# Kernel optimization log

Hardware: AMD Instinct MI355X
Metric: run time of the kernel (lower is better)

## Reference

```python
import jax, jax.numpy as jnp
import numpy as np

N_NODES = 40962
N_EDGES = 245760
K = 10  # gaussian kernels
D = 2   # pseudo-coordinate dim
EPS = 1e-15


def gmm_conv(x, edge_index, pseudo, g, mu, sigma, root, bias):
    """PyG GMMConv with aggr='mean', root_weight=True.
    x: [N, Cin], edge_index: [2, E] (row 0 = source j, row 1 = target i),
    pseudo: [E, D], g: [Cin, K*Cout], mu/sigma: [K, D], root: [Cin, Cout], bias: [Cout].
    """
    src, dst = edge_index[0], edge_index[1]
    E = pseudo.shape[0]
    # Gaussian mixture edge weights: [E, K]
    diff = pseudo[:, None, :] - mu[None, :, :]                     # [E, K, D]
    w = jnp.exp(jnp.sum(-0.5 * diff * diff / (EPS + sigma[None] ** 2), axis=-1))
    xj = x[src]                                                    # [E, Cin] gather
    y = (xj @ g).reshape(E, K, -1)                                 # [E, K, Cout]
    msg = jnp.sum(y * w[:, :, None], axis=1)                       # [E, Cout]
    agg = jax.ops.segment_sum(msg, dst, num_segments=N_NODES)      # scatter-add
    deg = jax.ops.segment_sum(jnp.ones((E,), x.dtype), dst, num_segments=N_NODES)
    agg = agg / jnp.maximum(deg, 1.0)[:, None]                     # mean aggregation
    return agg + x @ root + bias


def setup_inputs() -> dict:
    key = jax.random.key(0)
    ks = jax.random.split(key, 20)
    Cin, Ch, Cout = 64, 64, 128
    sc = lambda fan: 1.0 / np.sqrt(fan)
    inp = {
        "x": jax.random.normal(ks[0], (N_NODES, Cin), jnp.float32),
        "edge_index": jax.random.randint(ks[1], (2, N_EDGES), 0, N_NODES, jnp.int32),
        "pseudo": jax.random.uniform(ks[2], (N_EDGES, D), jnp.float32),
        # conv1: Cin -> Ch
        "g1": jax.random.normal(ks[3], (Cin, K * Ch), jnp.float32) * sc(Cin),
        "mu1": jax.random.uniform(ks[4], (K, D), jnp.float32),
        "sigma1": jax.random.uniform(ks[5], (K, D), jnp.float32) + 0.5,
        "root1": jax.random.normal(ks[6], (Cin, Ch), jnp.float32) * sc(Cin),
        "b1": jnp.zeros((Ch,), jnp.float32),
        # conv2: Ch -> Cout
        "g2": jax.random.normal(ks[7], (Ch, K * Cout), jnp.float32) * sc(Ch),
        "mu2": jax.random.uniform(ks[8], (K, D), jnp.float32),
        "sigma2": jax.random.uniform(ks[9], (K, D), jnp.float32) + 0.5,
        "root2": jax.random.normal(ks[10], (Ch, Cout), jnp.float32) * sc(Ch),
        "b2": jnp.zeros((Cout,), jnp.float32),
        # shortcut: Cin -> Cout (size_in != size_out)
        "gs": jax.random.normal(ks[11], (Cin, K * Cout), jnp.float32) * sc(Cin),
        "mus": jax.random.uniform(ks[12], (K, D), jnp.float32),
        "sigmas": jax.random.uniform(ks[13], (K, D), jnp.float32) + 0.5,
        "roots": jax.random.normal(ks[14], (Cin, Cout), jnp.float32) * sc(Cin),
        "bs": jnp.zeros((Cout,), jnp.float32),
    }
    return inp


def reference(x, edge_index, pseudo, g1, mu1, sigma1, root1, b1,
              g2, mu2, sigma2, root2, b2, gs, mus, sigmas, roots, bs):
    h = gmm_conv(x, edge_index, pseudo, g1, mu1, sigma1, root1, b1)
    h = jax.nn.relu(h)
    y = gmm_conv(h, edge_index, pseudo, g2, mu2, sigma2, root2, b2)
    x_s = gmm_conv(x, edge_index, pseudo, gs, mus, sigmas, roots, bs)
    return jax.nn.relu(y + x_s)
```

## Files before the change

### kernel.cpp

```cpp
#include <hip/hip_runtime.h>
#include <hip/hip_bf16.h>

using bf16 = __hip_bfloat16;
typedef __attribute__((ext_vector_type(8))) short short8;
typedef __attribute__((ext_vector_type(4))) float float4v;

#define N_NODES 40962
#define N_EDGES 245760
#define NP      41024
#define KG      10
#define SCAN_B  256
#define NBLK    ((NP + SCAN_B - 1) / SCAN_B)
#define GRID1   (NP / 64)

#define CVT_V   (N_NODES * 64 / 8)
#define CVT_BLK ((CVT_V + 255) / 256)
#define W3_BLK  (N_EDGES / 256)
#define PACK_N  (64 * 704 + 2 * 128 * 704)
#define PACK_BLK (PACK_N / 256)


__device__ __forceinline__ float ldf(const void* p, size_t i, int isf32) {
    return isf32 ? ((const float*)p)[i] : __bfloat162float(((const bf16*)p)[i]);
}
__device__ __forceinline__ float blo(unsigned u) { return __uint_as_float(u << 16); }
__device__ __forceinline__ float bhi(unsigned u) { return __uint_as_float(u & 0xffff0000u); }
__device__ __forceinline__ unsigned pk2(float a, float b) {
    union { bf16 h[2]; unsigned u; } t;
    t.h[0] = __float2bfloat16(a);
    t.h[1] = __float2bfloat16(b);
    return t.u;
}
__device__ __forceinline__ int rfl(int v) { return __builtin_amdgcn_readfirstlane(v); }

__global__ void k_detect_count(const void* x, const int* __restrict__ ei,
                               int* __restrict__ flag, int* __restrict__ deg) {
    if (blockIdx.x == 0) {
        __shared__ int huge_c, zero_even;
        if (threadIdx.x == 0) { huge_c = 0; zero_even = 0; }
        __syncthreads();
        const bf16* xb = (const bf16*)x;
        int lh = 0, lz = 0;
        for (int i = threadIdx.x; i < 8192; i += 256) {
            float v = __bfloat162float(xb[i]);
            if (!(fabsf(v) <= 1e4f)) lh++;
            if ((i & 1) == 0 && v == 0.0f) lz++;
        }
        atomicAdd(&huge_c, lh);
        atomicAdd(&zero_even, lz);
        __syncthreads();
        if (threadIdx.x == 0) flag[0] = (huge_c > 0 || zero_even > 3000) ? 1 : 0;
    } else {
        int e = (blockIdx.x - 1) * 256 + threadIdx.x;
        if (e < N_EDGES) atomicAdd(&deg[ei[N_EDGES + e]], 1);
    }
}

__global__ void k_scan1(const int* __restrict__ deg, int* __restrict__ offs,
                        int* __restrict__ bsum) {
    __shared__ int buf[SCAN_B];
    int t = threadIdx.x, b = blockIdx.x;
    int i = b * SCAN_B + t;
    int v = (i < NP) ? deg[i] : 0;
    buf[t] = v;
    __syncthreads();
    for (int off = 1; off < SCAN_B; off <<= 1) {
        int a = (t >= off) ? buf[t - off] : 0;
        __syncthreads();
        buf[t] += a;
        __syncthreads();
    }
    if (i < NP) offs[i] = buf[t] - v;
    if (t == SCAN_B - 1) bsum[b] = buf[t];
}

__global__ void k_scan3m(int* __restrict__ offs, const int* __restrict__ bsum,
                         const int* __restrict__ deg, int* __restrict__ cur,
                         float* __restrict__ invdeg) {
    __shared__ int buf[256];
    int t = threadIdx.x, b = blockIdx.x;
    int v = (t < NBLK) ? bsum[t] : 0;
    buf[t] = v;
    __syncthreads();
    for (int off = 1; off < 256; off <<= 1) {
        int a = (t >= off) ? buf[t - off] : 0;
        __syncthreads();
        buf[t] += a;
        __syncthreads();
    }
    int bofs = (b > 0) ? buf[b - 1] : 0;
    int total = buf[NBLK - 1];
    int i = b * 256 + t;
    if (i < NP) {
        int o = offs[i] + bofs;
        offs[i] = o;
        cur[i] = o;
        int d = deg[i];
        invdeg[i] = 1.0f / (float)(d > 1 ? d : 1);
    }
    if (i == 0) offs[NP] = total;
}

__global__ void k_fill(const int* __restrict__ ei, int* __restrict__ cur,
                       int* __restrict__ csr) {
    int e = blockIdx.x * 256 + threadIdx.x;
    if (e < N_EDGES) {
        int pos = atomicAdd(&cur[ei[N_EDGES + e]], 1);
        csr[pos] = e;
    }
}

__device__ __forceinline__ void gw_one(float p0, float p1, const void* mu,
                                       const void* sg, int f, float* out) {
#pragma unroll
    for (int k = 0; k < KG; k++) {
        float m0 = ldf(mu, 2 * k + 0, f), m1 = ldf(mu, 2 * k + 1, f);
        float s0 = ldf(sg, 2 * k + 0, f), s1 = ldf(sg, 2 * k + 1, f);
        float d0 = p0 - m0, d1 = p1 - m1;
        float t = -0.5f * (d0 * d0 / (1e-15f + s0 * s0) + d1 * d1 / (1e-15f + s1 * s1));
        out[k] = __expf(t);
    }
}

__device__ __forceinline__ void pack_frag(const void* g, const void* root, int f,
                                          int idx, int Cout, bf16* Bp) {
    int j = idx & 7;
    int lane = (idx >> 3) & 63;
    int rem = idx >> 9;
    int kc = rem % 22;
    int n = rem / 22;
    int col = n * 16 + (lane & 15);
    int k = kc * 32 + (lane >> 4) * 8 + j;
    float v;
    if (k < 512) {
        int cin = k >> 3, kg = k & 7;
        v = ldf(g, (size_t)cin * (KG * Cout) + (size_t)kg * Cout + col, f);
    } else if (k < 640) {
        int jj = k - 512;
        int cin = jj >> 1, kg = 8 + (jj & 1);
        v = ldf(g, (size_t)cin * (KG * Cout) + (size_t)kg * Cout + col, f);
    } else {
        v = ldf(root, (size_t)(k - 640) * Cout + col, f);
    }
    Bp[idx] = __float2bfloat16(v);
}

__global__ void k_prep_all(const void* __restrict__ x, const void* __restrict__ pseudo,
                           const void* mu1, const void* sg1, const void* mu2,
                           const void* sg2, const void* mus, const void* sgs,
                           const void* g1, const void* root1, const void* g2,
                           const void* root2, const void* gs, const void* roots,
                           const int* __restrict__ flag, bf16* __restrict__ Xf,
                           bf16* __restrict__ wab, bf16* __restrict__ w2b,
                           bf16* wt1p, bf16* wt2p, bf16* wtsp) {
    int b = blockIdx.x;
    int tid = threadIdx.x;
    int f = flag[0];
    if (b < CVT_BLK) {
        int i = b * 256 + tid;
        if (i < CVT_V) {
            int node = i >> 3, j = i & 7;
            uint4 u;
            if (f) {
                const float4* xf = (const float4*)x;
                float4 a = xf[2 * i], c = xf[2 * i + 1];
                union { bf16 t[8]; uint4 u; } tt;
                tt.t[0] = __float2bfloat16(a.x); tt.t[1] = __float2bfloat16(a.y);
                tt.t[2] = __float2bfloat16(a.z); tt.t[3] = __float2bfloat16(a.w);
                tt.t[4] = __float2bfloat16(c.x); tt.t[5] = __float2bfloat16(c.y);
                tt.t[6] = __float2bfloat16(c.z); tt.t[7] = __float2bfloat16(c.w);
                u = tt.u;
            } else {
                u = ((const uint4*)x)[i];
            }
            *(uint4*)(Xf + ((size_t)(j >> 2) * NP + node) * 32 + (j & 3) * 8) = u;
        }
    } else if (b < CVT_BLK + W3_BLK) {
        int e = (b - CVT_BLK) * 256 + tid;
        float p0 = ldf(pseudo, (size_t)e * 2 + 0, f);
        float p1 = ldf(pseudo, (size_t)e * 2 + 1, f);
        float o1[KG], o2[KG], os[KG];
        gw_one(p0, p1, mu1, sg1, f, o1);
        gw_one(p0, p1, mu2, sg2, f, o2);
        gw_one(p0, p1, mus, sgs, f, os);
        unsigned* d = (unsigned*)(wab + (size_t)e * 20);
        d[0] = pk2(o1[0], o1[1]); d[1] = pk2(o1[2], o1[3]);
        d[2] = pk2(o1[4], o1[5]); d[3] = pk2(o1[6], o1[7]);
        d[4] = pk2(o1[8], o1[9]);
        d[5] = pk2(os[0], os[1]); d[6] = pk2(os[2], os[3]);
        d[7] = pk2(os[4], os[5]); d[8] = pk2(os[6], os[7]);
        d[9] = pk2(os[8], os[9]);
        unsigned* d2 = (unsigned*)(w2b + (size_t)e * 10);
        d2[0] = pk2(o2[0], o2[1]); d2[1] = pk2(o2[2], o2[3]);
        d2[2] = pk2(o2[4], o2[5]); d2[3] = pk2(o2[6], o2[7]);
        d2[4] = pk2(o2[8], o2[9]);
    } else {
        int idx = (b - CVT_BLK - W3_BLK) * 256 + tid;
        if (idx < 64 * 704) {
            pack_frag(g1, root1, f, idx, 64, wt1p);
        } else if (idx < 64 * 704 + 128 * 704) {
            pack_frag(g2, root2, f, idx - 64 * 704, 128, wt2p);
        } else {
            pack_frag(gs, roots, f, idx - 64 * 704 - 128 * 704, 128, wtsp);
        }
    }
}

__device__ __forceinline__ void store_zf(bf16* Zf, int wid, int lane, const float* a,
                                         float inv) {
    union { bf16 h[8]; uint4 u; } p;
#pragma unroll
    for (int k = 0; k < 8; k++) p.h[k] = __float2bfloat16(a[k] * inv);
    *(uint4*)(Zf + ((size_t)(lane >> 2) * NP + wid) * 32 + (lane & 3) * 8) = p.u;
    *(unsigned*)(Zf + ((size_t)(16 + (lane >> 4)) * NP + wid) * 32 + (lane & 15) * 2) =
        pk2(a[8] * inv, a[9] * inv);
}

__device__ __forceinline__ float ldx_frag(const bf16* X, int src, int lane) {
    return __bfloat162float(X[((size_t)(lane >> 5) * NP + src) * 32 + (lane & 31)]);
}

__device__ __forceinline__ int csr_at(const int* csr, int idx) {
    if (idx > N_EDGES - 1) idx = N_EDGES - 1;
    return rfl(csr[idx]);
}

__global__ void k_gather2(const int* __restrict__ ei, const int* __restrict__ offs,
                          const int* __restrict__ csr, const bf16* __restrict__ wab,
                          const float* __restrict__ invdeg, const bf16* __restrict__ X,
                          bf16* __restrict__ Za, bf16* __restrict__ Zb) {
    int wid = (blockIdx.x * 256 + threadIdx.x) >> 6;
    int lane = threadIdx.x & 63;
    if (wid >= NP) return;
    float aa[KG], ab[KG];
#pragma unroll
    for (int k = 0; k < KG; k++) { aa[k] = 0.0f; ab[k] = 0.0f; }
    int beg = rfl(offs[wid]);
    int end = rfl(offs[wid + 1]);
    int cnt = end - beg;

    int e0 = csr_at(csr, beg + 0);
    int e1 = csr_at(csr, beg + 1);
    int e2 = csr_at(csr, beg + 2);
    int s1 = rfl(ei[e1]);
    const unsigned* wp0 = (const unsigned*)(wab + (size_t)e0 * 20);
    unsigned c0 = wp0[0], c1 = wp0[1], c2 = wp0[2], c3 = wp0[3], c4 = wp0[4];
    unsigned c5 = wp0[5], c6 = wp0[6], c7 = wp0[7], c8 = wp0[8], c9 = wp0[9];
    const unsigned* wp1 = (const unsigned*)(wab + (size_t)e1 * 20);
    unsigned n0 = wp1[0], n1 = wp1[1], n2 = wp1[2], n3 = wp1[3], n4 = wp1[4];
    unsigned n5 = wp1[5], n6 = wp1[6], n7 = wp1[7], n8 = wp1[8], n9 = wp1[9];
    int s0 = rfl(ei[e0]);
    float xv = ldx_frag(X, s0, lane);

    for (int t = 0; t < cnt; ++t) {
        int e3 = csr_at(csr, beg + t + 3);
        int s2 = rfl(ei[e2]);
        const unsigned* wp2 = (const unsigned*)(wab + (size_t)e2 * 20);
        unsigned m0 = wp2[0], m1 = wp2[1], m2 = wp2[2], m3 = wp2[3], m4 = wp2[4];
        unsigned m5 = wp2[5], m6 = wp2[6], m7 = wp2[7], m8 = wp2[8], m9 = wp2[9];
        float xv1 = ldx_frag(X, s1, lane);
        aa[0] += blo(c0) * xv; aa[1] += bhi(c0) * xv;
        aa[2] += blo(c1) * xv; aa[3] += bhi(c1) * xv;
        aa[4] += blo(c2) * xv; aa[5] += bhi(c2) * xv;
        aa[6] += blo(c3) * xv; aa[7] += bhi(c3) * xv;
        aa[8] += blo(c4) * xv; aa[9] += bhi(c4) * xv;
        ab[0] += blo(c5) * xv; ab[1] += bhi(c5) * xv;
        ab[2] += blo(c6) * xv; ab[3] += bhi(c6) * xv;
        ab[4] += blo(c7) * xv; ab[5] += bhi(c7) * xv;
        ab[6] += blo(c8) * xv; ab[7] += bhi(c8) * xv;
        ab[8] += blo(c9) * xv; ab[9] += bhi(c9) * xv;
        e2 = e3; s1 = s2; xv = xv1;
        c0 = n0; c1 = n1; c2 = n2; c3 = n3; c4 = n4;
        c5 = n5; c6 = n6; c7 = n7; c8 = n8; c9 = n9;
        n0 = m0; n1 = m1; n2 = m2; n3 = m3; n4 = m4;
        n5 = m5; n6 = m6; n7 = m7; n8 = m8; n9 = m9;
    }
    float inv = invdeg[wid];
    store_zf(Za, wid, lane, aa, inv);
    store_zf(Zb, wid, lane, ab, inv);
}

__global__ void k_gather(const int* __restrict__ ei, const int* __restrict__ offs,
                         const int* __restrict__ csr, const bf16* __restrict__ w,
                         int wstride, const float* __restrict__ invdeg,
                         const bf16* __restrict__ X, bf16* __restrict__ Z) {
    int wid = (blockIdx.x * 256 + threadIdx.x) >> 6;
    int lane = threadIdx.x & 63;
    if (wid >= NP) return;
    float acc[KG];
#pragma unroll
    for (int k = 0; k < KG; k++) acc[k] = 0.0f;
    int beg = rfl(offs[wid]);
    int end = rfl(offs[wid + 1]);
    int cnt = end - beg;

    int e0 = csr_at(csr, beg + 0);
    int e1 = csr_at(csr, beg + 1);
    int e2 = csr_at(csr, beg + 2);
    int s1 = rfl(ei[e1]);
    const unsigned* wp0 = (const unsigned*)(w + (size_t)e0 * wstride);
    unsigned c0 = wp0[0], c1 = wp0[1], c2 = wp0[2], c3 = wp0[3], c4 = wp0[4];
    const unsigned* wp1 = (const unsigned*)(w + (size_t)e1 * wstride);
    unsigned n0 = wp1[0], n1 = wp1[1], n2 = wp1[2], n3 = wp1[3], n4 = wp1[4];
    int s0 = rfl(ei[e0]);
    float xv = ldx_frag(X, s0, lane);

    for (int t = 0; t < cnt; ++t) {
        int e3 = csr_at(csr, beg + t + 3);
        int s2 = rfl(ei[e2]);
        const unsigned* wp2 = (const unsigned*)(w + (size_t)e2 * wstride);
        unsigned m0 = wp2[0], m1 = wp2[1], m2 = wp2[2], m3 = wp2[3], m4 = wp2[4];
        float xv1 = ldx_frag(X, s1, lane);
        acc[0] += blo(c0) * xv; acc[1] += bhi(c0) * xv;
        acc[2] += blo(c1) * xv; acc[3] += bhi(c1) * xv;
        acc[4] += blo(c2) * xv; acc[5] += bhi(c2) * xv;
        acc[6] += blo(c3) * xv; acc[7] += bhi(c3) * xv;
        acc[8] += blo(c4) * xv; acc[9] += bhi(c4) * xv;
        e2 = e3; s1 = s2; xv = xv1;
        c0 = n0; c1 = n1; c2 = n2; c3 = n3; c4 = n4;
        n0 = m0; n1 = m1; n2 = m2; n3 = m3; n4 = m4;
    }
    store_zf(Z, wid, lane, acc, invdeg[wid]);
}

template <int NT, int MODE>
__device__ __forceinline__ void gemm_body(
    int bid, const bf16* __restrict__ Zf, const bf16* __restrict__ Xf,
    const bf16* __restrict__ Bp, const void* __restrict__ bias, int f,
    const bf16* __restrict__ addsrc, bf16* __restrict__ outb,
    void* __restrict__ outp) {
    constexpr int Cout = NT * 16;
    constexpr int AD = (NT == 8) ? 2 : 4;
    int lane = threadIdx.x & 63;
    int wave = threadIdx.x >> 6;
    int m = lane & 15, quad = lane >> 4;
    int row0 = bid * 64 + wave * 16;

    const bf16* bbase = Bp + (size_t)lane * 8;
    const bf16* arow = Zf + ((size_t)(row0 + m)) * 32 + quad * 8;
    const bf16* xrow = Xf + ((size_t)(row0 + m)) * 32 + quad * 8;

    float4v acc[NT];
#pragma unroll
    for (int n = 0; n < NT; n++) acc[n] = (float4v){0.f, 0.f, 0.f, 0.f};

    short8 apre[AD];
#pragma unroll
    for (int i = 0; i < AD; i++)
        apre[i] = *(const short8*)(arow + (size_t)i * NP * 32);
    short8 bpre[2][NT];
#pragma unroll
    for (int n = 0; n < NT; n++) {
        bpre[0][n] = *(const short8*)(bbase + (size_t)(n * 22 + 0) * 512);
        bpre[1][n] = *(const short8*)(bbase + (size_t)(n * 22 + 1) * 512);
    }

#pragma unroll
    for (int kc = 0; kc < 22; kc++) {
        short8 a = apre[kc % AD];
        int kn = kc + AD;
        if (kn < 22) {
            apre[kc % AD] = (kn < 20)
                ? *(const short8*)(arow + (size_t)kn * NP * 32)
                : *(const short8*)(xrow + (size_t)(kn - 20) * NP * 32);
        }
        short8 bcur[NT];
#pragma unroll
        for (int n = 0; n < NT; n++) bcur[n] = bpre[kc & 1][n];
        if (kc + 2 < 22) {
#pragma unroll
            for (int n = 0; n < NT; n++)
                bpre[kc & 1][n] =
                    *(const short8*)(bbase + (size_t)(n * 22 + kc + 2) * 512);
        }
#pragma unroll
        for (int n = 0; n < NT; n++)
            acc[n] = __builtin_amdgcn_mfma_f32_16x16x32_bf16(a, bcur[n], acc[n], 0, 0, 0);
    }

#pragma unroll
    for (int n = 0; n < NT; n++) {
        int gcol = n * 16 + m;
        float bv = ldf(bias, gcol, f);
#pragma unroll
        for (int r = 0; r < 4; r++) {
            int grow = row0 + quad * 4 + r;
            if (grow >= N_NODES) continue;
            float v = acc[n][r] + bv;
            if (MODE == 0) {
                outb[((size_t)(gcol >> 5) * NP + grow) * 32 + (gcol & 31)] =
                    __float2bfloat16(fmaxf(v, 0.f));
            } else if (MODE == 1) {
                outb[(size_t)grow * Cout + gcol] = __float2bfloat16(v);
            } else {
                size_t oidx = (size_t)grow * Cout + gcol;
                v = fmaxf(v + __bfloat162float(addsrc[oidx]), 0.f);
                if (f) ((float*)outp)[oidx] = v;
                else   ((bf16*)outp)[oidx] = __float2bfloat16(v);
            }
        }
    }
}

__global__ __launch_bounds__(256) void k_gemm_pair(
    const bf16* __restrict__ za, const bf16* __restrict__ zb,
    const bf16* __restrict__ Xf, const bf16* __restrict__ wt1p,
    const bf16* __restrict__ wtsp, const void* __restrict__ b1,
    const void* __restrict__ bs, const int* __restrict__ flag,
    bf16* __restrict__ hf, bf16* __restrict__ ys) {
    int f = flag[0];
    if (blockIdx.x < GRID1)
        gemm_body<4, 0>(blockIdx.x, za, Xf, wt1p, b1, f, nullptr, hf, nullptr);
    else
        gemm_body<8, 1>(blockIdx.x - GRID1, zb, Xf, wtsp, bs, f, nullptr, ys, nullptr);
}

template <int NT, int MODE>
__global__ __launch_bounds__(256) void k_gemm_one(
    const bf16* __restrict__ Zf, const bf16* __restrict__ Xf,
    const bf16* __restrict__ Bp, const void* __restrict__ bias,
    const int* __restrict__ flag, const bf16* __restrict__ addsrc,
    bf16* __restrict__ outb, void* __restrict__ outp) {
    gemm_body<NT, MODE>(blockIdx.x, Zf, Xf, Bp, bias, flag[0], addsrc, outb, outp);
}

extern "C" void kernel_launch(void* const* d_in, const int* in_sizes, int n_in,
                              void* d_out, int out_size, void* d_ws, size_t ws_size,
                              hipStream_t stream) {
    const void* x      = d_in[0];
    const int*  ei     = (const int*)d_in[1];
    const void* pseudo = d_in[2];
    const void* g1     = d_in[3];
    const void* mu1    = d_in[4];
    const void* sg1    = d_in[5];
    const void* root1  = d_in[6];
    const void* b1     = d_in[7];
    const void* g2     = d_in[8];
    const void* mu2    = d_in[9];
    const void* sg2    = d_in[10];
    const void* root2  = d_in[11];
    const void* b2     = d_in[12];
    const void* gs     = d_in[13];
    const void* mus    = d_in[14];
    const void* sgs    = d_in[15];
    const void* roots  = d_in[16];
    const void* bs     = d_in[17];

    char* ws = (char*)d_ws;
    size_t off = 0;
    auto alloc = [&](size_t bytes) -> char* {
        char* p = ws + off;
        off += (bytes + 255) & ~(size_t)255;
        return p;
    };
    const size_t ZSZ = (size_t)20 * NP * 32 * 2;
    const size_t XFS = (size_t)2 * NP * 32 * 2;

    int*   flag   = (int*)alloc(256);
    int*   deg    = (int*)alloc((size_t)NP * 4);
    int*   offs   = (int*)alloc((size_t)(NP + 1) * 4);
    int*   cur    = (int*)alloc((size_t)NP * 4);
    float* invdeg = (float*)alloc((size_t)NP * 4);
    int*   bsum   = (int*)alloc((size_t)NBLK * 4);
    int*   csr    = (int*)alloc((size_t)N_EDGES * 4);
    bf16*  Xf     = (bf16*)alloc(XFS);
    bf16*  hf     = (bf16*)alloc(XFS);
    bf16*  ys     = (bf16*)alloc((size_t)N_NODES * 128 * 2);
    bf16*  wt1p   = (bf16*)alloc((size_t)64 * 704 * 2);
    bf16*  wt2p   = (bf16*)alloc((size_t)128 * 704 * 2);
    bf16*  wtsp   = (bf16*)alloc((size_t)128 * 704 * 2);
    bf16*  wab    = (bf16*)alloc((size_t)N_EDGES * 20 * 2);
    bf16*  w2b    = (bf16*)alloc((size_t)N_EDGES * 10 * 2);
    size_t common_end = off;

    bf16* za = (bf16*)alloc(ZSZ);
    bf16* zb = (bf16*)alloc(ZSZ);
    bool big = (off <= ws_size);

    hipMemsetAsync(deg, 0, (size_t)NP * 4, stream);
    k_detect_count<<<1 + (N_EDGES + 255) / 256, 256, 0, stream>>>(x, ei, flag, deg);
    k_prep_all<<<CVT_BLK + W3_BLK + PACK_BLK, 256, 0, stream>>>(
        x, pseudo, mu1, sg1, mu2, sg2, mus, sgs, g1, root1, g2, root2, gs, roots,
        flag, Xf, wab, w2b, wt1p, wt2p, wtsp);
    k_scan1<<<NBLK, SCAN_B, 0, stream>>>(deg, offs, bsum);
    k_scan3m<<<NBLK, 256, 0, stream>>>(offs, bsum, deg, cur, invdeg);
    k_fill<<<(N_EDGES + 255) / 256, 256, 0, stream>>>(ei, cur, csr);

    if (big) {
        k_gather2<<<NP / 4, 256, 0, stream>>>(ei, offs, csr, wab, invdeg, Xf, za, zb);
        k_gemm_pair<<<2 * GRID1, 256, 0, stream>>>(za, zb, Xf, wt1p, wtsp, b1, bs,
                                                   flag, hf, ys);
        k_gather<<<NP / 4, 256, 0, stream>>>(ei, offs, csr, w2b, 10, invdeg, hf, za);
        k_gemm_one<8, 2><<<GRID1, 256, 0, stream>>>(za, hf, wt2p, b2, flag, ys,
                                                    (bf16*)nullptr, d_out);
    } else {
        off = common_end;
        bf16* z = (bf16*)alloc(ZSZ);
        k_gather<<<NP / 4, 256, 0, stream>>>(ei, offs, csr, wab, 20, invdeg, Xf, z);
        k_gemm_one<4, 0><<<GRID1, 256, 0, stream>>>(z, Xf, wt1p, b1, flag,
                                                    (const bf16*)nullptr, hf, nullptr);
        k_gather<<<NP / 4, 256, 0, stream>>>(ei, offs, csr, wab + 10, 20, invdeg, Xf, z);
        k_gemm_one<8, 1><<<GRID1, 256, 0, stream>>>(z, Xf, wtsp, bs, flag,
                                                    (const bf16*)nullptr, ys, nullptr);
        k_gather<<<NP / 4, 256, 0, stream>>>(ei, offs, csr, w2b, 10, invdeg, hf, z);
        k_gemm_one<8, 2><<<GRID1, 256, 0, stream>>>(z, hf, wt2p, b2, flag, ys,
                                                    (bf16*)nullptr, d_out);
    }
}
```

Measured before the change: 294.2 us.

## Stage GEMM weight fragments through LDS via global_load_lds double buffering

The weight (B) fragments, previously loaded by every wave straight from global memory into registers, are now loaded once per block into a double-buffered LDS tile using global_load_lds, split across the four waves. Each k-step then reads B from LDS and prefetches the next chunk. This cuts redundant global and L2 traffic for B and lowers register pressure. In exchange it adds a block-wide barrier on every k-step and shortens the A prefetch depth from 2–4 steps to a single step.

```diff
diff --git a/kernel.cpp b/kernel.cpp
--- a/kernel.cpp
+++ b/kernel.cpp
@@ -32,6 +32,12 @@
     return t.u;
 }
 __device__ __forceinline__ int rfl(int v) { return __builtin_amdgcn_readfirstlane(v); }
+
+__device__ __forceinline__ void gll16(const void* g, void* l) {
+    __builtin_amdgcn_global_load_lds(
+        (const __attribute__((address_space(1))) void*)g,
+        (__attribute__((address_space(3))) void*)l, 16, 0, 0);
+}
 
 __global__ void k_detect_count(const void* x, const int* __restrict__ ei,
                                int* __restrict__ flag, int* __restrict__ deg) {
@@ -328,15 +334,13 @@
     int bid, const bf16* __restrict__ Zf, const bf16* __restrict__ Xf,
     const bf16* __restrict__ Bp, const void* __restrict__ bias, int f,
     const bf16* __restrict__ addsrc, bf16* __restrict__ outb,
-    void* __restrict__ outp) {
+    void* __restrict__ outp, bf16* __restrict__ sB) {
     constexpr int Cout = NT * 16;
-    constexpr int AD = (NT == 8) ? 2 : 4;
     int lane = threadIdx.x & 63;
     int wave = threadIdx.x >> 6;
     int m = lane & 15, quad = lane >> 4;
     int row0 = bid * 64 + wave * 16;
 
-    const bf16* bbase = Bp + (size_t)lane * 8;
     const bf16* arow = Zf + ((size_t)(row0 + m)) * 32 + quad * 8;
     const bf16* xrow = Xf + ((size_t)(row0 + m)) * 32 + quad * 8;
 
@@ -344,38 +348,34 @@
 #pragma unroll
     for (int n = 0; n < NT; n++) acc[n] = (float4v){0.f, 0.f, 0.f, 0.f};
 
-    short8 apre[AD];
-#pragma unroll
-    for (int i = 0; i < AD; i++)
-        apre[i] = *(const short8*)(arow + (size_t)i * NP * 32);
-    short8 bpre[2][NT];
-#pragma unroll
-    for (int n = 0; n < NT; n++) {
-        bpre[0][n] = *(const short8*)(bbase + (size_t)(n * 22 + 0) * 512);
-        bpre[1][n] = *(const short8*)(bbase + (size_t)(n * 22 + 1) * 512);
-    }
+#pragma unroll
+    for (int n = wave; n < NT; n += 4)
+        gll16(Bp + ((size_t)(n * 22 + 0) * 64 + lane) * 8, sB + n * 512);
+    short8 a_cur = *(const short8*)arow;
+    __syncthreads();
 
 #pragma unroll
     for (int kc = 0; kc < 22; kc++) {
-        short8 a = apre[kc % AD];
-        int kn = kc + AD;
-        if (kn < 22) {
-            apre[kc % AD] = (kn < 20)
+        int buf = kc & 1;
+        short8 a_nxt;
+        if (kc < 21) {
+            int kn = kc + 1;
+#pragma unroll
+            for (int n = wave; n < NT; n += 4)
+                gll16(Bp + ((size_t)(n * 22 + kn) * 64 + lane) * 8,
+                      sB + (size_t)(1 - buf) * NT * 512 + n * 512);
+            a_nxt = (kn < 20)
                 ? *(const short8*)(arow + (size_t)kn * NP * 32)
                 : *(const short8*)(xrow + (size_t)(kn - 20) * NP * 32);
         }
-        short8 bcur[NT];
-#pragma unroll
-        for (int n = 0; n < NT; n++) bcur[n] = bpre[kc & 1][n];
-        if (kc + 2 < 22) {
-#pragma unroll
-            for (int n = 0; n < NT; n++)
-                bpre[kc & 1][n] =
-                    *(const short8*)(bbase + (size_t)(n * 22 + kc + 2) * 512);
+        const bf16* bb = sB + (size_t)buf * NT * 512 + lane * 8;
+#pragma unroll
+        for (int n = 0; n < NT; n++) {
+            short8 b = *(const short8*)(bb + (size_t)n * 512);
+            acc[n] = __builtin_amdgcn_mfma_f32_16x16x32_bf16(a_cur, b, acc[n], 0, 0, 0);
         }
-#pragma unroll
-        for (int n = 0; n < NT; n++)
-            acc[n] = __builtin_amdgcn_mfma_f32_16x16x32_bf16(a, bcur[n], acc[n], 0, 0, 0);
+        __syncthreads();
+        if (kc < 21) a_cur = a_nxt;
     }
 
 #pragma unroll
@@ -408,11 +408,13 @@
     const bf16* __restrict__ wtsp, const void* __restrict__ b1,
     const void* __restrict__ bs, const int* __restrict__ flag,
     bf16* __restrict__ hf, bf16* __restrict__ ys) {
+    __shared__ bf16 sB[2 * 8 * 512];
     int f = flag[0];
     if (blockIdx.x < GRID1)
-        gemm_body<4, 0>(blockIdx.x, za, Xf, wt1p, b1, f, nullptr, hf, nullptr);
+        gemm_body<4, 0>(blockIdx.x, za, Xf, wt1p, b1, f, nullptr, hf, nullptr, sB);
     else
-        gemm_body<8, 1>(blockIdx.x - GRID1, zb, Xf, wtsp, bs, f, nullptr, ys, nullptr);
+        gemm_body<8, 1>(blockIdx.x - GRID1, zb, Xf, wtsp, bs, f, nullptr, ys, nullptr,
+                        sB);
 }
 
 template <int NT, int MODE>
@@ -421,7 +423,8 @@
     const bf16* __restrict__ Bp, const void* __restrict__ bias,
     const int* __restrict__ flag, const bf16* __restrict__ addsrc,
     bf16* __restrict__ outb, void* __restrict__ outp) {
-    gemm_body<NT, MODE>(blockIdx.x, Zf, Xf, Bp, bias, flag[0], addsrc, outb, outp);
+    __shared__ bf16 sB[2 * NT * 512];
+    gemm_body<NT, MODE>(blockIdx.x, Zf, Xf, Bp, bias, flag[0], addsrc, outb, outp, sB);
 }
 
 extern "C" void kernel_launch(void* const* d_in, const int* in_sizes, int n_in,
```

Result: faster. 274.7 us (-6.6%).
